# Kernel optimization log

Hardware: AMD Instinct MI355X
Metric: run time of the kernel (lower is better)

The kernel has to match this reference:

```python
import jax, jax.numpy as jnp
import numpy as np

B, C, L, D = 8, 256, 2048, 128  # batch, in_channels, seq_len, n_factor


def setup_inputs() -> dict:
    key = jax.random.key(0)
    ks = jax.random.split(key, 8)
    s = 1.0 / np.sqrt(C)
    return {
        "x_inner": jax.random.normal(ks[0], (B, C, L), jnp.float32),
        "x_outer": jax.random.normal(ks[1], (B, C, L), jnp.float32),
        "Wq": jax.random.normal(ks[2], (D, C), jnp.float32) * s,
        "bq": jax.random.normal(ks[3], (D,), jnp.float32) * 0.01,
        "Wk": jax.random.normal(ks[4], (D, C), jnp.float32) * s,
        "bk": jax.random.normal(ks[5], (D,), jnp.float32) * 0.01,
        "Wv": jax.random.normal(ks[6], (D, C), jnp.float32) * s,
        "bv": jax.random.normal(ks[7], (D,), jnp.float32) * 0.01,
    }


def reference(x_inner, x_outer, Wq, bq, Wk, bk, Wv, bv):
    # kernel-size-1 Conv1d == per-position linear over channels; permute -> [B, L, D]
    q = jnp.einsum('bcl,dc->bld', x_inner, Wq) + bq  # [B, Lq, D]
    k = jnp.einsum('bcl,dc->bld', x_outer, Wk) + bk  # [B, Lk, D]
    v = jnp.einsum('bcl,dc->bld', x_outer, Wv) + bv  # [B, Lk, D]
    scores = jnp.einsum('bqd,bkd->bqk', q, k) / jnp.sqrt(jnp.asarray(D, q.dtype))
    attn = jax.nn.softmax(scores, axis=2)            # [B, Lq, Lk]
    return jnp.einsum('bqk,bkd->bqd', attn, v)       # [B, Lq, D]
```

## Files before the change

### kernel.cpp

```cpp
#include <hip/hip_runtime.h>
#include <hip/hip_bf16.h>

#define NB 8
#define NC 256
#define NL 2048
#define ND 128
#define NROWS (NB * NL)
#define QKV_ELEMS ((size_t)NB * NL * ND)
#define W_ELEMS (ND * NC)
#define XS_STRIDE 264

typedef __attribute__((ext_vector_type(8))) short bf16x8;
typedef __attribute__((ext_vector_type(4))) float f32x4;
typedef __attribute__((ext_vector_type(16))) float f32x16;
typedef __attribute__((ext_vector_type(4))) unsigned int u32x4;

__device__ __forceinline__ unsigned short f2bf(float f) {
    union { float f; unsigned u; } v; v.f = f;
    unsigned r = v.u + 0x7fffu + ((v.u >> 16) & 1u);
    return (unsigned short)(r >> 16);
}

__device__ __forceinline__ unsigned cvt_pk_bf16(float lo, float hi) {
    unsigned r;
    asm("v_cvt_pk_bf16_f32 %0, %1, %2" : "=v"(r) : "v"(lo), "v"(hi));
    return r;
}

__device__ __forceinline__ void pl32swap(unsigned &a, unsigned &b) {
    asm("v_permlane32_swap_b32 %0, %1" : "+v"(a), "+v"(b));
}

__device__ __forceinline__ void load_lds16(const unsigned short* g, unsigned short* l) {
    __builtin_amdgcn_global_load_lds((const __attribute__((address_space(1))) unsigned int*)g,
                                     (__attribute__((address_space(3))) unsigned int*)l, 16, 0, 0);
}

__global__ void cast_w3(const float* __restrict__ wq, const float* __restrict__ wk,
                        const float* __restrict__ wv, unsigned short* __restrict__ dst) {
    int i = blockIdx.x * blockDim.x + threadIdx.x;
    if (i >= 3 * W_ELEMS) return;
    int sel = i / W_ELEMS, off = i - sel * W_ELEMS;
    const float* s = (sel == 0) ? wq : (sel == 1) ? wk : wv;
    dst[i] = f2bf(s[off]);
}

__device__ __forceinline__ int xs_col(int row, int col) {
    return col ^ (((row >> 2) & 7) << 3);
}

__device__ __forceinline__ void qk_project(const unsigned short* xs, const unsigned short* Wb,
                                           const float* bias, unsigned short* out,
                                           int b, int l0, int wave, int ln, int quad) {
    int m0w = wave * 16;
    f32x4 acc[8] = {};
    int rowq = m0w + ln;
    #pragma unroll
    for (int s = 0; s < 8; s++) {
        bf16x8 af = *reinterpret_cast<const bf16x8*>(xs + rowq * XS_STRIDE + xs_col(rowq, s * 32 + quad * 8));
        #pragma unroll
        for (int t = 0; t < 8; t++) {
            bf16x8 bfr = *reinterpret_cast<const bf16x8*>(Wb + (size_t)(t * 16 + ln) * NC + s * 32 + quad * 8);
            acc[t] = __builtin_amdgcn_mfma_f32_16x16x32_bf16(af, bfr, acc[t], 0, 0, 0);
        }
    }
    #pragma unroll
    for (int t = 0; t < 8; t++) {
        int col = t * 16 + ln;
        float bi = bias[col];
        #pragma unroll
        for (int r = 0; r < 4; r++)
            out[(size_t)(b * NL + l0 + m0w + quad * 4 + r) * ND + col] = f2bf(acc[t][r] + bi);
    }
}

__global__ __launch_bounds__(256, 4) void proj_direct(const float* __restrict__ xi,
                                                      const float* __restrict__ xo,
                                                      const unsigned short* __restrict__ Wall,
                                                      const float* __restrict__ bq,
                                                      const float* __restrict__ bk,
                                                      const float* __restrict__ bv,
                                                      unsigned short* __restrict__ Qb,
                                                      unsigned short* __restrict__ Kb,
                                                      unsigned short* __restrict__ Vtb) {
    __shared__ unsigned short xs[64 * XS_STRIDE];
    int b = blockIdx.x >> 5, lt = blockIdx.x & 31, l0 = lt * 64;
    int y = blockIdx.y;
    int wave = threadIdx.x >> 6, lane = threadIdx.x & 63;
    int ln = lane & 15, quad = lane >> 4;

    const float* xsrc = (y == 0 ? xi : xo) + (size_t)b * NC * NL + l0;
    int l4 = ln * 4;
    #pragma unroll
    for (int G = 0; G < 4; G++) {
        int c0 = G * 64 + wave * 16 + quad * 4;
        float4 r[4];
        #pragma unroll
        for (int cc = 0; cc < 4; cc++)
            r[cc] = *reinterpret_cast<const float4*>(xsrc + (size_t)(c0 + cc) * NL + l4);
        #pragma unroll
        for (int k = 0; k < 4; k++) {
            int row = l4 + k;
            const float* f0 = reinterpret_cast<const float*>(&r[0]);
            const float* f1 = reinterpret_cast<const float*>(&r[1]);
            const float* f2 = reinterpret_cast<const float*>(&r[2]);
            const float* f3 = reinterpret_cast<const float*>(&r[3]);
            uint2 w2 = { cvt_pk_bf16(f0[k], f1[k]), cvt_pk_bf16(f2[k], f3[k]) };
            *reinterpret_cast<uint2*>(&xs[row * XS_STRIDE + xs_col(row, c0)]) = w2;
        }
    }
    __syncthreads();

    if (y == 0) {
        qk_project(xs, Wall, bq, Qb, b, l0, wave, ln, quad);
    } else {
        qk_project(xs, Wall + W_ELEMS, bk, Kb, b, l0, wave, ln, quad);
        const unsigned short* Wb = Wall + 2 * (size_t)W_ELEMS;
        f32x4 acc[2][4] = {};
        #pragma unroll
        for (int s = 0; s < 8; s++) {
            bf16x8 wf0 = *reinterpret_cast<const bf16x8*>(Wb + (size_t)(wave * 32 + ln) * NC + s * 32 + quad * 8);
            bf16x8 wf1 = *reinterpret_cast<const bf16x8*>(Wb + (size_t)(wave * 32 + 16 + ln) * NC + s * 32 + quad * 8);
            #pragma unroll
            for (int t = 0; t < 4; t++) {
                int rowv = t * 16 + ln;
                bf16x8 xb = *reinterpret_cast<const bf16x8*>(xs + rowv * XS_STRIDE + xs_col(rowv, s * 32 + quad * 8));
                acc[0][t] = __builtin_amdgcn_mfma_f32_16x16x32_bf16(wf0, xb, acc[0][t], 0, 0, 0);
                acc[1][t] = __builtin_amdgcn_mfma_f32_16x16x32_bf16(wf1, xb, acc[1][t], 0, 0, 0);
            }
        }
        #pragma unroll
        for (int u = 0; u < 2; u++)
            #pragma unroll
            for (int t = 0; t < 4; t++)
                #pragma unroll
                for (int r = 0; r < 4; r++) {
                    int d = wave * 32 + u * 16 + quad * 4 + r;
                    Vtb[(size_t)(b * ND + d) * NL + l0 + t * 16 + ln] = f2bf(acc[u][t][r] + bv[d]);
                }
    }
}

__global__ __launch_bounds__(256) void flash_attn_fused(const unsigned short* __restrict__ Q,
                                                        const unsigned short* __restrict__ K,
                                                        const unsigned short* __restrict__ Vt,
                                                        float* __restrict__ out) {
    __shared__ unsigned short kbuf[2][64 * 128];
    __shared__ unsigned short vbuf[2][128 * 64];
    int bx = blockIdx.x;
    bx = ((bx & 7) << 5) | (bx >> 3);
    int b = bx >> 5, qt = bx & 31;
    int q0 = qt * 64;
    int wave = threadIdx.x >> 6, lane = threadIdx.x & 63;
    int l31 = lane & 31, h = lane >> 5;
    int qg = wave >> 1, half = wave & 1;
    const float scale = 0.08838834764831845f * 1.4426950408889634f;

    bf16x8 qf[8];
    const unsigned short* qrow = Q + (size_t)(b * NL + q0 + qg * 32 + l31) * ND + h * 8;
    #pragma unroll
    for (int s = 0; s < 8; s++) qf[s] = *reinterpret_cast<const bf16x8*>(qrow + s * 16);

    float lsum = 0.f;
    f32x16 o_acc[4] = {};

    const unsigned short* kg = K + (size_t)b * NL * ND;
    const unsigned short* vg = Vt + (size_t)b * ND * NL;

    int krt = wave * 16 + (lane >> 4);
    int kjs = (lane & 15);
    int vdt = wave * 32 + (lane >> 3);
    int vjs = (lane & 7);

    #pragma unroll
    for (int i = 0; i < 4; i++) {
        int rt = krt + i * 4;
        load_lds16(kg + (size_t)rt * ND + (kjs ^ (rt & 15)) * 8, kbuf[0] + (wave * 16 + i * 4) * 128);
    }
    #pragma unroll
    for (int i = 0; i < 4; i++) {
        int dt = vdt + i * 8;
        load_lds16(vg + (size_t)dt * NL + (vjs ^ (dt & 7)) * 8, vbuf[0] + (wave * 32 + i * 8) * 64);
    }

    const int niter = NL >> 6;
    for (int it = 0; it < niter; it++) {
        int cur = it & 1;
        __syncthreads();

        if (it + 1 < niter) {
            int kt = (it + 1) * 64;
            int nxt = cur ^ 1;
            #pragma unroll
            for (int i = 0; i < 4; i++) {
                int rt = krt + i * 4;
                load_lds16(kg + (size_t)(kt + rt) * ND + (kjs ^ (rt & 15)) * 8, kbuf[nxt] + (wave * 16 + i * 4) * 128);
            }
            #pragma unroll
            for (int i = 0; i < 4; i++) {
                int dt = vdt + i * 8;
                load_lds16(vg + (size_t)dt * NL + kt + (vjs ^ (dt & 7)) * 8, vbuf[nxt] + (wave * 32 + i * 8) * 64);
            }
        }
        const unsigned short* kb = kbuf[cur];
        const unsigned short* vb = vbuf[cur];

        f32x16 sacc = {};
        __builtin_amdgcn_s_setprio(1);
        {
            const unsigned short* krow_p = kb + (half * 32 + l31) * 128;
            #pragma unroll
            for (int s = 0; s < 8; s++) {
                bf16x8 kf = *reinterpret_cast<const bf16x8*>(krow_p + (((s * 2 + h) ^ (l31 & 15)) << 3));
                sacc = __builtin_amdgcn_mfma_f32_32x32x16_bf16(kf, qf[s], sacc, 0, 0, 0);
            }
        }
        __builtin_amdgcn_s_setprio(0);

        float p[16];
        #pragma unroll
        for (int g = 0; g < 16; g++) p[g] = __builtin_exp2f(sacc[g] * scale);
        lsum += (((p[0] + p[1]) + (p[2] + p[3])) + ((p[4] + p[5]) + (p[6] + p[7])))
              + (((p[8] + p[9]) + (p[10] + p[11])) + ((p[12] + p[13]) + (p[14] + p[15])));
        unsigned c0 = cvt_pk_bf16(p[0], p[1]),   c1 = cvt_pk_bf16(p[2], p[3]);
        unsigned c2 = cvt_pk_bf16(p[4], p[5]),   c3 = cvt_pk_bf16(p[6], p[7]);
        unsigned c4 = cvt_pk_bf16(p[8], p[9]),   c5 = cvt_pk_bf16(p[10], p[11]);
        unsigned c6 = cvt_pk_bf16(p[12], p[13]), c7 = cvt_pk_bf16(p[14], p[15]);
        pl32swap(c0, c2); pl32swap(c1, c3);
        pl32swap(c4, c6); pl32swap(c5, c7);
        u32x4 wlo = {c0, c1, c2, c3};
        u32x4 whi = {c4, c5, c6, c7};
        bf16x8 pb0 = __builtin_bit_cast(bf16x8, wlo);
        bf16x8 pb1 = __builtin_bit_cast(bf16x8, whi);

        __builtin_amdgcn_s_setprio(1);
        #pragma unroll
        for (int dt = 0; dt < 4; dt++) {
            const unsigned short* vrow = vb + (dt * 32 + l31) * 64;
            int s0 = half * 2;
            bf16x8 vf0 = *reinterpret_cast<const bf16x8*>(vrow + ((((s0 + 0) * 2 + h) ^ (l31 & 7)) << 3));
            bf16x8 vf1 = *reinterpret_cast<const bf16x8*>(vrow + ((((s0 + 1) * 2 + h) ^ (l31 & 7)) << 3));
            o_acc[dt] = __builtin_amdgcn_mfma_f32_32x32x16_bf16(vf0, pb0, o_acc[dt], 0, 0, 0);
            o_acc[dt] = __builtin_amdgcn_mfma_f32_32x32x16_bf16(vf1, pb1, o_acc[dt], 0, 0, 0);
        }
        __builtin_amdgcn_s_setprio(0);
    }
    lsum += __shfl_xor(lsum, 32);

    __syncthreads();
    float* ored = reinterpret_cast<float*>(&kbuf[0][0]);
    float* lred = reinterpret_cast<float*>(&vbuf[0][0]);
    if (half == 1) {
        float* o = ored + qg * (128 * 32);
        #pragma unroll
        for (int dt = 0; dt < 4; dt++)
            #pragma unroll
            for (int g = 0; g < 4; g++)
                #pragma unroll
                for (int r = 0; r < 4; r++)
                    o[(dt * 32 + g * 8 + h * 4 + r) * 32 + l31] = o_acc[dt][g * 4 + r];
        if (lane < 32) lred[qg * 32 + l31] = lsum;
    }
    __syncthreads();
    if (half == 0) {
        float* o = ored + qg * (128 * 32);
        float Lt = lsum + lred[qg * 32 + l31];
        float inv = 1.0f / Lt;
        int qrow_g = b * NL + q0 + qg * 32 + l31;
        #pragma unroll
        for (int dt = 0; dt < 4; dt++) {
            #pragma unroll
            for (int g = 0; g < 4; g++) {
                f32x4 v4;
                #pragma unroll
                for (int r = 0; r < 4; r++)
                    v4[r] = (o_acc[dt][g * 4 + r] + o[(dt * 32 + g * 8 + h * 4 + r) * 32 + l31]) * inv;
                *reinterpret_cast<f32x4*>(out + (size_t)qrow_g * ND + dt * 32 + g * 8 + h * 4) = v4;
            }
        }
    }
}

extern "C" void kernel_launch(void* const* d_in, const int* in_sizes, int n_in,
                              void* d_out, int out_size, void* d_ws, size_t ws_size,
                              hipStream_t stream) {
    const float* x_inner = (const float*)d_in[0];
    const float* x_outer = (const float*)d_in[1];
    const float* Wq = (const float*)d_in[2];
    const float* bq = (const float*)d_in[3];
    const float* Wk = (const float*)d_in[4];
    const float* bk = (const float*)d_in[5];
    const float* Wv = (const float*)d_in[6];
    const float* bv = (const float*)d_in[7];
    float* out = (float*)d_out;

    char* w = (char*)d_ws;
    unsigned short* Qb = (unsigned short*)w;
    unsigned short* Kb = Qb + QKV_ELEMS;
    unsigned short* Vtb = Kb + QKV_ELEMS;
    unsigned short* Wall = Vtb + QKV_ELEMS;

    cast_w3<<<(3 * W_ELEMS + 255) / 256, 256, 0, stream>>>(Wq, Wk, Wv, Wall);
    dim3 pgrid(NB * (NL / 64), 2);
    proj_direct<<<pgrid, 256, 0, stream>>>(x_inner, x_outer, Wall, bq, bk, bv, Qb, Kb, Vtb);
    flash_attn_fused<<<NB * (NL / 64), 256, 0, stream>>>(Qb, Kb, Vtb, out);
}
```

Measured before the change: 159.2 us.

## Split KV dimension across two blocks per query tile and merge partials

Splits each query tile's key/value range into two halves processed by separate blocks, doubling the grid and adding a launch bound of two blocks per CU. Each block writes unnormalized partial outputs and row sums to workspace, and a new merge kernel sums them and normalizes. The QK^T accumulation also uses two independent MFMA accumulators to break the dependency chain. This trades extra global traffic and an extra launch for better CU occupancy and latency hiding.

```diff
diff --git a/kernel.cpp b/kernel.cpp
--- a/kernel.cpp
+++ b/kernel.cpp
@@ -141,16 +141,20 @@
     }
 }
 
-__global__ __launch_bounds__(256) void flash_attn_fused(const unsigned short* __restrict__ Q,
+__global__ __launch_bounds__(256, 2) void flash_attn_s2(const unsigned short* __restrict__ Q,
                                                         const unsigned short* __restrict__ K,
                                                         const unsigned short* __restrict__ Vt,
-                                                        float* __restrict__ out) {
+                                                        float* __restrict__ Opart,
+                                                        float* __restrict__ lbuf,
+                                                        int kvlen) {
     __shared__ unsigned short kbuf[2][64 * 128];
     __shared__ unsigned short vbuf[2][128 * 64];
     int bx = blockIdx.x;
     bx = ((bx & 7) << 5) | (bx >> 3);
     int b = bx >> 5, qt = bx & 31;
     int q0 = qt * 64;
+    int sp = blockIdx.y;
+    int kv0 = sp * kvlen;
     int wave = threadIdx.x >> 6, lane = threadIdx.x & 63;
     int l31 = lane & 31, h = lane >> 5;
     int qg = wave >> 1, half = wave & 1;
@@ -175,21 +179,21 @@
     #pragma unroll
     for (int i = 0; i < 4; i++) {
         int rt = krt + i * 4;
-        load_lds16(kg + (size_t)rt * ND + (kjs ^ (rt & 15)) * 8, kbuf[0] + (wave * 16 + i * 4) * 128);
+        load_lds16(kg + (size_t)(kv0 + rt) * ND + (kjs ^ (rt & 15)) * 8, kbuf[0] + (wave * 16 + i * 4) * 128);
     }
     #pragma unroll
     for (int i = 0; i < 4; i++) {
         int dt = vdt + i * 8;
-        load_lds16(vg + (size_t)dt * NL + (vjs ^ (dt & 7)) * 8, vbuf[0] + (wave * 32 + i * 8) * 64);
-    }
-
-    const int niter = NL >> 6;
+        load_lds16(vg + (size_t)dt * NL + kv0 + (vjs ^ (dt & 7)) * 8, vbuf[0] + (wave * 32 + i * 8) * 64);
+    }
+
+    int niter = kvlen >> 6;
     for (int it = 0; it < niter; it++) {
         int cur = it & 1;
         __syncthreads();
 
         if (it + 1 < niter) {
-            int kt = (it + 1) * 64;
+            int kt = kv0 + (it + 1) * 64;
             int nxt = cur ^ 1;
             #pragma unroll
             for (int i = 0; i < 4; i++) {
@@ -205,21 +209,23 @@
         const unsigned short* kb = kbuf[cur];
         const unsigned short* vb = vbuf[cur];
 
-        f32x16 sacc = {};
+        f32x16 sacc0 = {}, sacc1 = {};
         __builtin_amdgcn_s_setprio(1);
         {
             const unsigned short* krow_p = kb + (half * 32 + l31) * 128;
             #pragma unroll
-            for (int s = 0; s < 8; s++) {
-                bf16x8 kf = *reinterpret_cast<const bf16x8*>(krow_p + (((s * 2 + h) ^ (l31 & 15)) << 3));
-                sacc = __builtin_amdgcn_mfma_f32_32x32x16_bf16(kf, qf[s], sacc, 0, 0, 0);
+            for (int s = 0; s < 8; s += 2) {
+                bf16x8 kf0 = *reinterpret_cast<const bf16x8*>(krow_p + ((((s + 0) * 2 + h) ^ (l31 & 15)) << 3));
+                bf16x8 kf1 = *reinterpret_cast<const bf16x8*>(krow_p + ((((s + 1) * 2 + h) ^ (l31 & 15)) << 3));
+                sacc0 = __builtin_amdgcn_mfma_f32_32x32x16_bf16(kf0, qf[s], sacc0, 0, 0, 0);
+                sacc1 = __builtin_amdgcn_mfma_f32_32x32x16_bf16(kf1, qf[s + 1], sacc1, 0, 0, 0);
             }
         }
         __builtin_amdgcn_s_setprio(0);
 
         float p[16];
         #pragma unroll
-        for (int g = 0; g < 16; g++) p[g] = __builtin_exp2f(sacc[g] * scale);
+        for (int g = 0; g < 16; g++) p[g] = __builtin_exp2f((sacc0[g] + sacc1[g]) * scale);
         lsum += (((p[0] + p[1]) + (p[2] + p[3])) + ((p[4] + p[5]) + (p[6] + p[7])))
               + (((p[8] + p[9]) + (p[10] + p[11])) + ((p[12] + p[13]) + (p[14] + p[15])));
         unsigned c0 = cvt_pk_bf16(p[0], p[1]),   c1 = cvt_pk_bf16(p[2], p[3]);
@@ -265,8 +271,9 @@
     if (half == 0) {
         float* o = ored + qg * (128 * 32);
         float Lt = lsum + lred[qg * 32 + l31];
-        float inv = 1.0f / Lt;
         int qrow_g = b * NL + q0 + qg * 32 + l31;
+        if (lane < 32) lbuf[(size_t)sp * NROWS + qrow_g] = Lt;
+        float* op = Opart + (size_t)sp * QKV_ELEMS;
         #pragma unroll
         for (int dt = 0; dt < 4; dt++) {
             #pragma unroll
@@ -274,11 +281,29 @@
                 f32x4 v4;
                 #pragma unroll
                 for (int r = 0; r < 4; r++)
-                    v4[r] = (o_acc[dt][g * 4 + r] + o[(dt * 32 + g * 8 + h * 4 + r) * 32 + l31]) * inv;
-                *reinterpret_cast<f32x4*>(out + (size_t)qrow_g * ND + dt * 32 + g * 8 + h * 4) = v4;
-            }
-        }
-    }
+                    v4[r] = o_acc[dt][g * 4 + r] + o[(dt * 32 + g * 8 + h * 4 + r) * 32 + l31];
+                *reinterpret_cast<f32x4*>(op + (size_t)qrow_g * ND + dt * 32 + g * 8 + h * 4) = v4;
+            }
+        }
+    }
+}
+
+__global__ __launch_bounds__(256) void attn_merge(const float* __restrict__ Opart,
+                                                  const float* __restrict__ lbuf,
+                                                  float* __restrict__ out, int S) {
+    int idx = blockIdx.x * 256 + threadIdx.x;
+    int row = idx >> 5;
+    int dg = (idx & 31) * 4;
+    float L = 0.f;
+    float4 acc = make_float4(0.f, 0.f, 0.f, 0.f);
+    for (int s = 0; s < S; s++) {
+        L += lbuf[(size_t)s * NROWS + row];
+        float4 o = *reinterpret_cast<const float4*>(Opart + (size_t)s * QKV_ELEMS + (size_t)row * ND + dg);
+        acc.x += o.x; acc.y += o.y; acc.z += o.z; acc.w += o.w;
+    }
+    float inv = 1.0f / L;
+    float4 res = make_float4(acc.x * inv, acc.y * inv, acc.z * inv, acc.w * inv);
+    *reinterpret_cast<float4*>(out + (size_t)row * ND + dg) = res;
 }
 
 extern "C" void kernel_launch(void* const* d_in, const int* in_sizes, int n_in,
@@ -294,8 +319,12 @@
     const float* bv = (const float*)d_in[7];
     float* out = (float*)d_out;
 
+    const int S = 2;
     char* w = (char*)d_ws;
-    unsigned short* Qb = (unsigned short*)w;
+    float* Opart = (float*)w;
+    float* lbuf = (float*)(w + (size_t)S * QKV_ELEMS * 4);
+    char* w2 = w + (size_t)S * QKV_ELEMS * 4 + (size_t)S * NROWS * 4;
+    unsigned short* Qb = (unsigned short*)w2;
     unsigned short* Kb = Qb + QKV_ELEMS;
     unsigned short* Vtb = Kb + QKV_ELEMS;
     unsigned short* Wall = Vtb + QKV_ELEMS;
@@ -303,5 +332,7 @@
     cast_w3<<<(3 * W_ELEMS + 255) / 256, 256, 0, stream>>>(Wq, Wk, Wv, Wall);
     dim3 pgrid(NB * (NL / 64), 2);
     proj_direct<<<pgrid, 256, 0, stream>>>(x_inner, x_outer, Wall, bq, bk, bv, Qb, Kb, Vtb);
-    flash_attn_fused<<<NB * (NL / 64), 256, 0, stream>>>(Qb, Kb, Vtb, out);
-}
+    dim3 fgrid(NB * (NL / 64), S);
+    flash_attn_s2<<<fgrid, 256, 0, stream>>>(Qb, Kb, Vtb, Opart, lbuf, NL / S);
+    attn_merge<<<(NROWS * ND / 4 + 255) / 256, 256, 0, stream>>>(Opart, lbuf, out, S);
+}
```

Measured after the change: 149.0 us. 1.07x faster.

## Split KV sequence across two wave groups in 512-thread attention blocks

Applied to the files above, without the earlier changes.

The attention kernel now launches 512 threads per block. Two groups of four waves each process half of the key/value sequence, each with its own double-buffered LDS tiles (128 KB of shared memory). Partial outputs and row sums from three of the four wave slots are reduced through LDS at the end. The QK MFMA chain is also split into two independent accumulators to shorten the dependency chain. This raises per-block parallelism and latency hiding within the same 256-block grid, at the cost of a larger final reduction and limiting occupancy to one block per CU.

```diff
diff --git a/kernel.cpp b/kernel.cpp
--- a/kernel.cpp
+++ b/kernel.cpp
@@ -5,7 +5,6 @@
 #define NC 256
 #define NL 2048
 #define ND 128
-#define NROWS (NB * NL)
 #define QKV_ELEMS ((size_t)NB * NL * ND)
 #define W_ELEMS (ND * NC)
 #define XS_STRIDE 264
@@ -141,19 +140,22 @@
     }
 }
 
-__global__ __launch_bounds__(256) void flash_attn_fused(const unsigned short* __restrict__ Q,
-                                                        const unsigned short* __restrict__ K,
-                                                        const unsigned short* __restrict__ Vt,
-                                                        float* __restrict__ out) {
-    __shared__ unsigned short kbuf[2][64 * 128];
-    __shared__ unsigned short vbuf[2][128 * 64];
+__global__ __launch_bounds__(512, 1) void flash_attn_one(const unsigned short* __restrict__ Q,
+                                                         const unsigned short* __restrict__ K,
+                                                         const unsigned short* __restrict__ Vt,
+                                                         float* __restrict__ out) {
+    __shared__ __align__(16) unsigned short smem[65536];
+    unsigned short* kbufp = smem;
+    unsigned short* vbufp = smem + 2 * 2 * 64 * 128;
     int bx = blockIdx.x;
     bx = ((bx & 7) << 5) | (bx >> 3);
     int b = bx >> 5, qt = bx & 31;
     int q0 = qt * 64;
     int wave = threadIdx.x >> 6, lane = threadIdx.x & 63;
     int l31 = lane & 31, h = lane >> 5;
-    int qg = wave >> 1, half = wave & 1;
+    int sp = wave >> 2, wave4 = wave & 3;
+    int qg = wave4 >> 1, half = wave4 & 1;
+    int kv0 = sp * (NL / 2);
     const float scale = 0.08838834764831845f * 1.4426950408889634f;
 
     bf16x8 qf[8];
@@ -167,59 +169,67 @@
     const unsigned short* kg = K + (size_t)b * NL * ND;
     const unsigned short* vg = Vt + (size_t)b * ND * NL;
 
-    int krt = wave * 16 + (lane >> 4);
+    int krt = wave4 * 16 + (lane >> 4);
     int kjs = (lane & 15);
-    int vdt = wave * 32 + (lane >> 3);
+    int vdt = wave4 * 32 + (lane >> 3);
     int vjs = (lane & 7);
 
-    #pragma unroll
-    for (int i = 0; i < 4; i++) {
-        int rt = krt + i * 4;
-        load_lds16(kg + (size_t)rt * ND + (kjs ^ (rt & 15)) * 8, kbuf[0] + (wave * 16 + i * 4) * 128);
-    }
-    #pragma unroll
-    for (int i = 0; i < 4; i++) {
-        int dt = vdt + i * 8;
-        load_lds16(vg + (size_t)dt * NL + (vjs ^ (dt & 7)) * 8, vbuf[0] + (wave * 32 + i * 8) * 64);
-    }
-
-    const int niter = NL >> 6;
+    {
+        unsigned short* kb0 = kbufp + (sp * 2 + 0) * (64 * 128);
+        unsigned short* vb0 = vbufp + (sp * 2 + 0) * (128 * 64);
+        #pragma unroll
+        for (int i = 0; i < 4; i++) {
+            int rt = krt + i * 4;
+            load_lds16(kg + (size_t)(kv0 + rt) * ND + (kjs ^ (rt & 15)) * 8, kb0 + (wave4 * 16 + i * 4) * 128);
+        }
+        #pragma unroll
+        for (int i = 0; i < 4; i++) {
+            int dt = vdt + i * 8;
+            load_lds16(vg + (size_t)dt * NL + kv0 + (vjs ^ (dt & 7)) * 8, vb0 + (wave4 * 32 + i * 8) * 64);
+        }
+    }
+
+    const int niter = (NL / 2) >> 6;
     for (int it = 0; it < niter; it++) {
         int cur = it & 1;
         __syncthreads();
 
         if (it + 1 < niter) {
-            int kt = (it + 1) * 64;
+            int kt = kv0 + (it + 1) * 64;
             int nxt = cur ^ 1;
+            unsigned short* kbn = kbufp + (sp * 2 + nxt) * (64 * 128);
+            unsigned short* vbn = vbufp + (sp * 2 + nxt) * (128 * 64);
             #pragma unroll
             for (int i = 0; i < 4; i++) {
                 int rt = krt + i * 4;
-                load_lds16(kg + (size_t)(kt + rt) * ND + (kjs ^ (rt & 15)) * 8, kbuf[nxt] + (wave * 16 + i * 4) * 128);
+                load_lds16(kg + (size_t)(kt + rt) * ND + (kjs ^ (rt & 15)) * 8, kbn + (wave4 * 16 + i * 4) * 128);
             }
             #pragma unroll
             for (int i = 0; i < 4; i++) {
                 int dt = vdt + i * 8;
-                load_lds16(vg + (size_t)dt * NL + kt + (vjs ^ (dt & 7)) * 8, vbuf[nxt] + (wave * 32 + i * 8) * 64);
-            }
-        }
-        const unsigned short* kb = kbuf[cur];
-        const unsigned short* vb = vbuf[cur];
-
-        f32x16 sacc = {};
+                load_lds16(vg + (size_t)dt * NL + kt + (vjs ^ (dt & 7)) * 8, vbn + (wave4 * 32 + i * 8) * 64);
+            }
+        }
+        const unsigned short* kb = kbufp + (sp * 2 + cur) * (64 * 128);
+        const unsigned short* vb = vbufp + (sp * 2 + cur) * (128 * 64);
+
+        f32x16 sacc0 = {}, sacc1 = {};
         __builtin_amdgcn_s_setprio(1);
         {
             const unsigned short* krow_p = kb + (half * 32 + l31) * 128;
             #pragma unroll
-            for (int s = 0; s < 8; s++) {
-                bf16x8 kf = *reinterpret_cast<const bf16x8*>(krow_p + (((s * 2 + h) ^ (l31 & 15)) << 3));
-                sacc = __builtin_amdgcn_mfma_f32_32x32x16_bf16(kf, qf[s], sacc, 0, 0, 0);
+            for (int s = 0; s < 8; s += 2) {
+                bf16x8 kf0 = *reinterpret_cast<const bf16x8*>(krow_p + ((((s + 0) * 2 + h) ^ (l31 & 15)) << 3));
+                bf16x8 kf1 = *reinterpret_cast<const bf16x8*>(krow_p + ((((s + 1) * 2 + h) ^ (l31 & 15)) << 3));
+                sacc0 = __builtin_amdgcn_mfma_f32_32x32x16_bf16(kf0, qf[s], sacc0, 0, 0, 0);
+                sacc1 = __builtin_amdgcn_mfma_f32_32x32x16_bf16(kf1, qf[s + 1], sacc1, 0, 0, 0);
             }
         }
         __builtin_amdgcn_s_setprio(0);
 
         float p[16];
         #pragma unroll
-        for (int g = 0; g < 16; g++) p[g] = __builtin_exp2f(sacc[g] * scale);
+        for (int g = 0; g < 16; g++) p[g] = __builtin_exp2f((sacc0[g] + sacc1[g]) * scale);
         lsum += (((p[0] + p[1]) + (p[2] + p[3])) + ((p[4] + p[5]) + (p[6] + p[7])))
               + (((p[8] + p[9]) + (p[10] + p[11])) + ((p[12] + p[13]) + (p[14] + p[15])));
         unsigned c0 = cvt_pk_bf16(p[0], p[1]),   c1 = cvt_pk_bf16(p[2], p[3]);
@@ -248,10 +258,11 @@
     lsum += __shfl_xor(lsum, 32);
 
     __syncthreads();
-    float* ored = reinterpret_cast<float*>(&kbuf[0][0]);
-    float* lred = reinterpret_cast<float*>(&vbuf[0][0]);
-    if (half == 1) {
-        float* o = ored + qg * (128 * 32);
+    float* ored = reinterpret_cast<float*>(smem);
+    float* lred = reinterpret_cast<float*>(smem) + 2 * 3 * 128 * 32;
+    int idx = sp * 2 + half;
+    if (idx > 0) {
+        float* o = ored + (qg * 3 + (idx - 1)) * (128 * 32);
         #pragma unroll
         for (int dt = 0; dt < 4; dt++)
             #pragma unroll
@@ -259,22 +270,28 @@
                 #pragma unroll
                 for (int r = 0; r < 4; r++)
                     o[(dt * 32 + g * 8 + h * 4 + r) * 32 + l31] = o_acc[dt][g * 4 + r];
-        if (lane < 32) lred[qg * 32 + l31] = lsum;
+        if (lane < 32) lred[(qg * 3 + (idx - 1)) * 32 + l31] = lsum;
     }
     __syncthreads();
-    if (half == 0) {
-        float* o = ored + qg * (128 * 32);
-        float Lt = lsum + lred[qg * 32 + l31];
+    if (idx == 0) {
+        float Lt = lsum + lred[(qg * 3 + 0) * 32 + l31]
+                        + lred[(qg * 3 + 1) * 32 + l31]
+                        + lred[(qg * 3 + 2) * 32 + l31];
         float inv = 1.0f / Lt;
         int qrow_g = b * NL + q0 + qg * 32 + l31;
+        const float* o0 = ored + (qg * 3 + 0) * (128 * 32);
+        const float* o1 = ored + (qg * 3 + 1) * (128 * 32);
+        const float* o2 = ored + (qg * 3 + 2) * (128 * 32);
         #pragma unroll
         for (int dt = 0; dt < 4; dt++) {
             #pragma unroll
             for (int g = 0; g < 4; g++) {
                 f32x4 v4;
                 #pragma unroll
-                for (int r = 0; r < 4; r++)
-                    v4[r] = (o_acc[dt][g * 4 + r] + o[(dt * 32 + g * 8 + h * 4 + r) * 32 + l31]) * inv;
+                for (int r = 0; r < 4; r++) {
+                    int di = (dt * 32 + g * 8 + h * 4 + r) * 32 + l31;
+                    v4[r] = (o_acc[dt][g * 4 + r] + o0[di] + o1[di] + o2[di]) * inv;
+                }
                 *reinterpret_cast<f32x4*>(out + (size_t)qrow_g * ND + dt * 32 + g * 8 + h * 4) = v4;
             }
         }
@@ -303,5 +320,5 @@
     cast_w3<<<(3 * W_ELEMS + 255) / 256, 256, 0, stream>>>(Wq, Wk, Wv, Wall);
     dim3 pgrid(NB * (NL / 64), 2);
     proj_direct<<<pgrid, 256, 0, stream>>>(x_inner, x_outer, Wall, bq, bk, bv, Qb, Kb, Vtb);
-    flash_attn_fused<<<NB * (NL / 64), 256, 0, stream>>>(Qb, Kb, Vtb, out);
-}
+    flash_attn_one<<<NB * (NL / 64), 512, 0, stream>>>(Qb, Kb, Vtb, out);
+}
```

Measured after the change: 141.6 us. -11.1%, faster.
